# Kernel optimization log

Measured on AMD Instinct MI355X. Metric: run time of the kernel, lower is better.

Reference implementation:

```python
import jax, jax.numpy as jnp
import numpy as np

DIM = 1024
HEAD = 8
SPLIT = DIM // HEAD
EPS = 1e-6


def layernorm(x, gamma, beta):
    m = jnp.mean(x, axis=-1, keepdims=True)
    v = jnp.mean(jnp.square(x - m), axis=-1, keepdims=True)
    return (x - m) / jnp.sqrt(v + EPS) * gamma + beta


def setup_inputs() -> dict:
    key = jax.random.key(0)
    ks = jax.random.split(key, 6)
    s = 0.02
    return {
        "x": jax.random.normal(ks[0], (4, 2048, DIM), dtype=jnp.float32),
        "W_in": jax.random.normal(ks[1], (DIM, DIM), dtype=jnp.float32) * s,
        "gamma": jnp.ones((DIM,), jnp.float32),
        "beta": jnp.zeros((DIM,), jnp.float32),
        "Wq": jax.random.normal(ks[2], (HEAD, SPLIT, SPLIT), dtype=jnp.float32) * s,
        "Wk": jax.random.normal(ks[3], (HEAD, SPLIT, SPLIT), dtype=jnp.float32) * s,
        "Wv": jax.random.normal(ks[4], (HEAD, SPLIT, SPLIT), dtype=jnp.float32) * s,
        "Wf": jax.random.normal(ks[5], (DIM, DIM), dtype=jnp.float32) * s,
        "bf": jnp.zeros((DIM,), jnp.float32),
    }


def reference(x, W_in, gamma, beta, Wq, Wk, Wv, Wf, bf):
    B, S, _ = x.shape
    mod = x @ W_in  # [B,S,DIM], Dense no bias
    # pre-norm then split into heads: [B,S,HEAD,SPLIT]
    h = layernorm(mod, gamma, beta).reshape(B, S, HEAD, SPLIT)
    # per-head Q/K/V projections (batched over heads instead of Python loop)
    q = jnp.einsum('bshd,hde->bhse', h, Wq)
    k = jnp.einsum('bshd,hde->bhse', h, Wk)
    v = jnp.einsum('bshd,hde->bhse', h, Wv)
    # keras Attention(): unscaled dot-product scores (use_scale=False)
    scores = jnp.einsum('bhqe,bhke->bhqk', q, k)
    attn = jax.nn.softmax(scores, axis=-1)
    o = jnp.einsum('bhqk,bhke->bqhe', attn, v).reshape(B, S, DIM)
    mod = mod + o  # residual
    # FFN residual with shared LayerNorm params and ELU Dense
    mod = mod + jax.nn.elu(layernorm(mod, gamma, beta) @ Wf + bf)
    return mod
```

## Files before the change

kernel.cpp:

```cpp
#include <hip/hip_runtime.h>
#include <hip/hip_bf16.h>

#define DIMN 1024
#define NHEAD 8
#define ESPL 128
#define NB 4
#define SEQ 2048
#define NROWS (NB * SEQ)
#define LNEPS 1e-6f
#define L2E 1.442695041f

typedef unsigned short u16;
typedef unsigned int u32;
typedef __attribute__((ext_vector_type(8))) short short8;
typedef __attribute__((ext_vector_type(4))) short s16x4;
typedef __attribute__((ext_vector_type(4))) float f32x4;

__device__ __forceinline__ u16 f2bf(float f) {
  u32 u = __float_as_uint(f);
  u += 0x7FFFu + ((u >> 16) & 1u);
  return (u16)(u >> 16);
}

__device__ __forceinline__ u32 pk2bf(float a, float b) {
  u32 r;
  asm("v_cvt_pk_bf16_f32 %0, %1, %2" : "=v"(r) : "v"(a), "v"(b));
  return r;
}

__device__ __forceinline__ uint2 pack4bf(float4 v) {
  uint2 r;
  r.x = pk2bf(v.x, v.y);
  r.y = pk2bf(v.z, v.w);
  return r;
}

__device__ __forceinline__ float fexp2(float x) {
  float r;
  asm("v_exp_f32 %0, %1" : "=v"(r) : "v"(x));
  return r;
}

__device__ __forceinline__ float eluf(float x) { return x > 0.f ? x : expm1f(x); }

__device__ __forceinline__ void gl2lds16(const u16* g, u16* l) {
  __builtin_amdgcn_global_load_lds((const __attribute__((address_space(1))) u32*)g,
                                   (__attribute__((address_space(3))) u32*)l, 16, 0, 0);
}

__global__ __launch_bounds__(256) void ln_apply(const float* __restrict__ modp,
                                                const float* __restrict__ gamma,
                                                const float* __restrict__ beta,
                                                const float* __restrict__ s1p,
                                                const float* __restrict__ s2p,
                                                u16* __restrict__ outb) {
  int base = (blockIdx.x * 256 + threadIdx.x) * 4;
  int row = base >> 10, col = base & 1023;
  float s1 = s1p[row], s2 = s2p[row];
  float mu = s1 * (1.f / DIMN);
  float rsd = rsqrtf(fmaxf(s2 * (1.f / DIMN) - mu * mu, 0.f) + LNEPS);
  float4 v = *(const float4*)(modp + base);
  float4 g = *(const float4*)(gamma + col);
  float4 bb = *(const float4*)(beta + col);
  v.x = (v.x - mu) * rsd * g.x + bb.x;
  v.y = (v.y - mu) * rsd * g.y + bb.y;
  v.z = (v.z - mu) * rsd * g.z + bb.z;
  v.w = (v.w - mu) * rsd * g.w + bb.w;
  *(uint2*)(outb + base) = pack4bf(v);
}

__device__ __forceinline__ void wtrans_body(u16 (*tl)[68], const float* __restrict__ src,
                                            u16* __restrict__ dst, int K, int N, int n0,
                                            int k0) {
  const int t = threadIdx.x;
  const int r = t >> 2;
#pragma unroll
  for (int j = 0; j < 4; j++) {
    int f = (t & 3) + j * 4;
    float4 v = *(const float4*)(src + (size_t)(k0 + r) * N + n0 + f * 4);
    *(uint2*)&tl[r][f * 4] = pack4bf(v);
  }
  __syncthreads();
#pragma unroll
  for (int j = 0; j < 4; j++) {
    int f = (t & 3) + j * 4;
    ushort4 o;
    o.x = tl[f * 4 + 0][r];
    o.y = tl[f * 4 + 1][r];
    o.z = tl[f * 4 + 2][r];
    o.w = tl[f * 4 + 3][r];
    *(ushort4*)(dst + (size_t)(n0 + r) * K + k0 + f * 4) = o;
  }
}

__global__ __launch_bounds__(256) void prep_fused(
    const float* __restrict__ x, u16* __restrict__ xb, const float* __restrict__ W_in,
    u16* __restrict__ wt1, const float* __restrict__ Wf, u16* __restrict__ wt2,
    const float* __restrict__ Wq, const float* __restrict__ Wk, const float* __restrict__ Wv,
    u16* __restrict__ dq, u16* __restrict__ dk, u16* __restrict__ dv) {
  __shared__ u16 tl[64][68];
  const int bid = blockIdx.x;
  if (bid < NROWS) {
    int base = (bid * 256 + threadIdx.x) * 4;
    *(uint2*)(xb + base) = pack4bf(*(const float4*)(x + base));
  } else if (bid < NROWS + 512) {
    int z = bid - NROWS;
    const float* s = (z & 256) ? Wf : W_in;
    u16* d = (z & 256) ? wt2 : wt1;
    z &= 255;
    wtrans_body(tl, s, d, DIMN, DIMN, (z & 15) * 64, (z >> 4) * 64);
  } else {
    int z = bid - NROWS - 512;
    int xy = z & 3, zz = z >> 2;
    int mi = zz >> 3, hh = zz & 7;
    const float* s = (mi == 0) ? Wq : (mi == 1) ? Wk : Wv;
    u16* d = (mi == 0) ? dq : (mi == 1) ? dk : dv;
    s += (size_t)hh * ESPL * ESPL;
    d += (size_t)hh * ESPL * ESPL;
    wtrans_body(tl, s, d, ESPL, ESPL, (xy & 1) * 64, (xy >> 1) * 64);
  }
}

template <int MODE>
__global__ __launch_bounds__(256, 2) void gemm_bf16(
    const u16* __restrict__ A, const u16* __restrict__ Bt, const float* __restrict__ resid,
    const float* __restrict__ bias, float* __restrict__ s1p, float* __restrict__ s2p,
    float* __restrict__ C) {
  __shared__ __align__(16) char lds[65536];
  const int t = threadIdx.x;
  const int w = t >> 6, lane = t & 63, quad = lane >> 4, l16 = lane & 15;
  const int wm = w & 1, wn = w >> 1;
  const int lin = blockIdx.x + gridDim.x * blockIdx.y;
  const int xcd = lin & 7, slot = lin >> 3;
  const int m0 = (xcd * 8 + (slot >> 3)) * 128;
  const int n0 = (slot & 7) * 128;

  auto stage = [&](int koff, int bi) {
    const u16* ag = A + (size_t)m0 * DIMN + koff;
    const u16* bg = Bt + (size_t)n0 * DIMN + koff;
    u16* As = (u16*)(lds + bi * 32768);
    u16* Bs = (u16*)(lds + bi * 32768 + 16384);
#pragma unroll
    for (int i = 0; i < 4; i++) {
      int pbase = (w * 4 + i) * 64;
      int p = pbase + lane;
      int r = p >> 3, c8 = (p & 7) ^ (r & 7);
      gl2lds16(ag + (size_t)r * DIMN + c8 * 8, As + pbase * 8);
      gl2lds16(bg + (size_t)r * DIMN + c8 * 8, Bs + pbase * 8);
    }
  };

  f32x4 acc[4][4];
#pragma unroll
  for (int mt = 0; mt < 4; mt++)
#pragma unroll
    for (int nt = 0; nt < 4; nt++) acc[mt][nt] = (f32x4){0.f, 0.f, 0.f, 0.f};

  stage(0, 0);
  __syncthreads();
  for (int kt = 0; kt < DIMN / 64; kt++) {
    if (kt + 1 < DIMN / 64) stage((kt + 1) * 64, (kt + 1) & 1);
    const u16* As = (const u16*)(lds + (kt & 1) * 32768);
    const u16* Bs = (const u16*)(lds + (kt & 1) * 32768 + 16384);
#pragma unroll
    for (int ks = 0; ks < 2; ks++) {
      short8 af[4], bfr[4];
#pragma unroll
      for (int mt = 0; mt < 4; mt++) {
        int row = wm * 64 + mt * 16 + l16;
        int pc = (ks * 4 + quad) ^ (row & 7);
        af[mt] = *(const short8*)(As + row * 64 + pc * 8);
      }
#pragma unroll
      for (int nt = 0; nt < 4; nt++) {
        int row = wn * 64 + nt * 16 + l16;
        int pc = (ks * 4 + quad) ^ (row & 7);
        bfr[nt] = *(const short8*)(Bs + row * 64 + pc * 8);
      }
#pragma unroll
      for (int mt = 0; mt < 4; mt++)
#pragma unroll
        for (int nt = 0; nt < 4; nt++)
          acc[mt][nt] = __builtin_amdgcn_mfma_f32_16x16x32_bf16(bfr[nt], af[mt], acc[mt][nt], 0, 0, 0);
    }
    __syncthreads();
  }
#pragma unroll
  for (int mt = 0; mt < 4; mt++) {
    int row = m0 + wm * 64 + mt * 16 + l16;
    float s1 = 0.f, s2 = 0.f;
#pragma unroll
    for (int nt = 0; nt < 4; nt++) {
      int col = n0 + wn * 64 + nt * 16 + quad * 4;
      size_t off = (size_t)row * DIMN + col;
      f32x4 v = acc[mt][nt];
      if (MODE == 0) {
        *(f32x4*)(C + off) = v;
        s1 += (v[0] + v[1]) + (v[2] + v[3]);
        s2 += (v[0] * v[0] + v[1] * v[1]) + (v[2] * v[2] + v[3] * v[3]);
      } else {
        float4 rv = *(const float4*)(resid + off);
        float4 bv = *(const float4*)(bias + col);
        float4 o;
        o.x = rv.x + eluf(v[0] + bv.x);
        o.y = rv.y + eluf(v[1] + bv.y);
        o.z = rv.z + eluf(v[2] + bv.z);
        o.w = rv.w + eluf(v[3] + bv.w);
        *(float4*)(C + off) = o;
      }
    }
    if (MODE == 0) {
      s1 += __shfl_xor(s1, 16);
      s1 += __shfl_xor(s1, 32);
      s2 += __shfl_xor(s2, 16);
      s2 += __shfl_xor(s2, 32);
      if (quad == 0) {
        atomicAdd(s1p + row, s1);
        atomicAdd(s2p + row, s2);
      }
    }
  }
}

#define QP 136

__global__ __launch_bounds__(256) void qkv_mfma(
    const float* __restrict__ modp, const u16* __restrict__ wqt, const u16* __restrict__ wkt,
    const u16* __restrict__ wvt, const float* __restrict__ gamma, const float* __restrict__ beta,
    const float* __restrict__ s1p, const float* __restrict__ s2p, u16* __restrict__ qo,
    u16* __restrict__ ko, u16* __restrict__ vto) {
  __shared__ u16 Asl[128 * QP];
  __shared__ u16 Bsl[128 * QP];
  const int t = threadIdx.x;
  const int w = t >> 6, lane = t & 63, quad = lane >> 4, l16 = lane & 15;
  const int wm = w & 1, wn = w >> 1;
  const int lin = blockIdx.x + gridDim.x * blockIdx.y;
  const int xcd = lin & 7, slot = lin >> 3;
  const int s0 = (slot >> 2) * 128;
  const int bh = (slot & 3) * 8 + xcd;
  const int b = bh >> 3, hh = bh & 7;
  const int sr8 = t >> 3, sf8 = t & 7;
#pragma unroll
  for (int p = 0; p < 4; p++) {
    int r = sr8 + 32 * p;
    int rowg = b * SEQ + s0 + r;
    float s1 = s1p[rowg], s2 = s2p[rowg];
    float mu = s1 * (1.f / DIMN);
    float rsd = rsqrtf(fmaxf(s2 * (1.f / DIMN) - mu * mu, 0.f) + LNEPS);
    const float* ap = modp + (size_t)rowg * DIMN + hh * ESPL;
#pragma unroll
    for (int j = 0; j < 4; j++) {
      int f = sf8 + j * 8;
      float4 v = *(const float4*)(ap + f * 4);
      float4 g = *(const float4*)(gamma + hh * ESPL + f * 4);
      float4 bb = *(const float4*)(beta + hh * ESPL + f * 4);
      v.x = (v.x - mu) * rsd * g.x + bb.x;
      v.y = (v.y - mu) * rsd * g.y + bb.y;
      v.z = (v.z - mu) * rsd * g.z + bb.z;
      v.w = (v.w - mu) * rsd * g.w + bb.w;
      *(uint2*)(Asl + r * QP + f * 4) = pack4bf(v);
    }
  }
  __syncthreads();
  short8 afr[4][4];
#pragma unroll
  for (int k4 = 0; k4 < 4; k4++)
#pragma unroll
    for (int mt = 0; mt < 4; mt++)
      afr[k4][mt] = *(const short8*)(Asl + (wm * 64 + mt * 16 + l16) * QP + k4 * 32 + quad * 8);

  const u16* Ws[3] = {wqt, wkt, wvt};
  for (int mi = 0; mi < 3; mi++) {
    __syncthreads();
    const u16* wsrc = Ws[mi] + ((size_t)hh << 14);
#pragma unroll
    for (int p = 0; p < 4; p++) {
      int r = sr8 + 32 * p;
#pragma unroll
      for (int j = 0; j < 2; j++) {
        int f = sf8 + j * 8;
        *(uint4*)(Bsl + r * QP + f * 8) = *(const uint4*)(wsrc + r * ESPL + f * 8);
      }
    }
    __syncthreads();
    f32x4 acc[4][4];
#pragma unroll
    for (int mt = 0; mt < 4; mt++)
#pragma unroll
      for (int nt = 0; nt < 4; nt++) acc[mt][nt] = (f32x4){0.f, 0.f, 0.f, 0.f};
#pragma unroll
    for (int k4 = 0; k4 < 4; k4++) {
      short8 bfr[4];
#pragma unroll
      for (int nt = 0; nt < 4; nt++)
        bfr[nt] = *(const short8*)(Bsl + (wn * 64 + nt * 16 + l16) * QP + k4 * 32 + quad * 8);
      if (mi < 2) {
#pragma unroll
        for (int mt = 0; mt < 4; mt++)
#pragma unroll
          for (int nt = 0; nt < 4; nt++)
            acc[mt][nt] = __builtin_amdgcn_mfma_f32_16x16x32_bf16(bfr[nt], afr[k4][mt], acc[mt][nt], 0, 0, 0);
      } else {
#pragma unroll
        for (int mt = 0; mt < 4; mt++)
#pragma unroll
          for (int nt = 0; nt < 4; nt++)
            acc[mt][nt] = __builtin_amdgcn_mfma_f32_16x16x32_bf16(afr[k4][mt], bfr[nt], acc[mt][nt], 0, 0, 0);
      }
    }
    if (mi < 2) {
      u16* o = (mi == 0) ? qo : ko;
#pragma unroll
      for (int mt = 0; mt < 4; mt++) {
        int s = s0 + wm * 64 + mt * 16 + l16;
#pragma unroll
        for (int nt = 0; nt < 4; nt++) {
          int e0 = wn * 64 + nt * 16 + quad * 4;
          uint2 pk;
          pk.x = pk2bf(acc[mt][nt][0], acc[mt][nt][1]);
          pk.y = pk2bf(acc[mt][nt][2], acc[mt][nt][3]);
          *(uint2*)(o + ((size_t)bh * SEQ + s) * ESPL + e0) = pk;
        }
      }
    } else {
#pragma unroll
      for (int mt = 0; mt < 4; mt++)
#pragma unroll
        for (int nt = 0; nt < 4; nt++) {
          int e = wn * 64 + nt * 16 + l16;
          int sbase = s0 + wm * 64 + mt * 16 + quad * 4;
          uint2 pk;
          pk.x = pk2bf(acc[mt][nt][0], acc[mt][nt][1]);
          pk.y = pk2bf(acc[mt][nt][2], acc[mt][nt][3]);
          *(uint2*)(vto + ((size_t)bh * ESPL + e) * SEQ + sbase) = pk;
        }
    }
  }
}

#define OBP 132
#define RESCALE_THR 8.f

__global__ __launch_bounds__(256, 2) void attn_mfma(const u16* __restrict__ q,
                                                    const u16* __restrict__ kk,
                                                    const u16* __restrict__ vt,
                                                    float* __restrict__ modp,
                                                    float* __restrict__ s1p,
                                                    float* __restrict__ s2p) {
  __shared__ __align__(16) char lds[81920];
  const int t = threadIdx.x;
  const int w = t >> 6, lane = t & 63, quad = lane >> 4, l16 = lane & 15;
  const int lin = blockIdx.x + gridDim.x * blockIdx.y;
  const int xcd = lin & 7, slot = lin >> 3;
  const int qt = slot & 15;
  const int bh = xcd * 4 + (slot >> 4);
  const int b = bh >> 3, hh = bh & 7;
  const size_t qkbase = (size_t)bh * SEQ * ESPL;
  const int qrow0 = qt * 128 + w * 32;
  const u16* kg0 = kk + qkbase;
  const u16* vg0 = vt + qkbase;
  char* Pt = lds + 65536 + w * 4096;
  const int swz = (l16 & 7) << 4;

  short8 qf[2][4];
#pragma unroll
  for (int g = 0; g < 2; g++) {
    const u16* qrow = q + qkbase + (size_t)(qrow0 + g * 16 + l16) * ESPL + quad * 8;
#pragma unroll
    for (int kc = 0; kc < 4; kc++) qf[g][kc] = *(const short8*)(qrow + kc * 32);
  }

  float m_st[2] = {-1e30f, -1e30f}, l_st[2] = {0.f, 0.f};
  f32x4 oacc[2][8];
#pragma unroll
  for (int g = 0; g < 2; g++)
#pragma unroll
    for (int et = 0; et < 8; et++) oacc[g][et] = (f32x4){0.f, 0.f, 0.f, 0.f};

  auto stage = [&](int kt, int bi) {
    const u16* kg = kg0 + (size_t)kt * 64 * ESPL;
    const u16* vg = vg0 + (size_t)kt * 64;
    u16* Ksb = (u16*)(lds + bi * 32768);
    u16* Vsb = (u16*)(lds + bi * 32768 + 16384);
#pragma unroll
    for (int i = 0; i < 4; i++) {
      int pbase = w * 64 + i * 256;
      int p = pbase + lane;
      int r = p >> 4, c8 = (p & 15) ^ (r & 15);
      gl2lds16(kg + r * ESPL + c8 * 8, Ksb + pbase * 8);
      int e = p >> 3, v8 = (p & 7) ^ (e & 7);
      gl2lds16(vg + (size_t)e * SEQ + v8 * 8, Vsb + pbase * 8);
    }
  };

  stage(0, 0);
  __syncthreads();

  for (int kt = 0; kt < SEQ / 64; kt++) {
    if (kt + 1 < SEQ / 64) stage(kt + 1, (kt + 1) & 1);
    const u16* Ks = (const u16*)(lds + (kt & 1) * 32768);
    const u16* Vs = (const u16*)(lds + (kt & 1) * 32768 + 16384);
    f32x4 sacc[4][2];
#pragma unroll
    for (int mt = 0; mt < 4; mt++)
#pragma unroll
      for (int g = 0; g < 2; g++) sacc[mt][g] = (f32x4){0.f, 0.f, 0.f, 0.f};
    __builtin_amdgcn_s_setprio(1);
#pragma unroll
    for (int mt = 0; mt < 4; mt++) {
#pragma unroll
      for (int kc = 0; kc < 4; kc++) {
        short8 kf = *(const short8*)(Ks + (mt * 16 + l16) * 128 + (((kc * 4 + quad) ^ l16) << 3));
        sacc[mt][0] = __builtin_amdgcn_mfma_f32_16x16x32_bf16(kf, qf[0][kc], sacc[mt][0], 0, 0, 0);
        sacc[mt][1] = __builtin_amdgcn_mfma_f32_16x16x32_bf16(kf, qf[1][kc], sacc[mt][1], 0, 0, 0);
      }
    }
    __builtin_amdgcn_s_setprio(0);
    float alpha[2];
    bool updf[2];
#pragma unroll
    for (int g = 0; g < 2; g++) {
      const f32x4 a = sacc[0][g], b2 = sacc[1][g], c2 = sacc[2][g], d2 = sacc[3][g];
      float t0 = fmaxf(fmaxf(a[0], a[1]), a[2]);
      float t1 = fmaxf(fmaxf(a[3], b2[0]), b2[1]);
      float t2 = fmaxf(fmaxf(b2[2], b2[3]), c2[0]);
      float t3 = fmaxf(fmaxf(c2[1], c2[2]), c2[3]);
      float t4 = fmaxf(fmaxf(d2[0], d2[1]), d2[2]);
      float mloc = fmaxf(fmaxf(fmaxf(t0, t1), t2), fmaxf(fmaxf(t3, t4), d2[3]));
      mloc = fmaxf(mloc, __shfl_xor(mloc, 16));
      mloc = fmaxf(mloc, __shfl_xor(mloc, 32));
      updf[g] = !__all(mloc - m_st[g] <= RESCALE_THR);
      if (updf[g]) {
        float mnew = fmaxf(m_st[g], mloc);
        alpha[g] = fexp2((m_st[g] - mnew) * L2E);
        m_st[g] = mnew;
      } else {
        alpha[g] = 1.f;
      }
      const float mkn = -m_st[g] * L2E;
      float sum = 0.f;
#pragma unroll
      for (int mt = 0; mt < 4; mt++) {
        float p0 = fexp2(fmaf(sacc[mt][g][0], L2E, mkn));
        float p1 = fexp2(fmaf(sacc[mt][g][1], L2E, mkn));
        float p2 = fexp2(fmaf(sacc[mt][g][2], L2E, mkn));
        float p3 = fexp2(fmaf(sacc[mt][g][3], L2E, mkn));
        sum += (p0 + p1) + (p2 + p3);
        uint2 pkv = make_uint2(pk2bf(p0, p1), pk2bf(p2, p3));
        *(uint2*)(Pt + g * 2048 + l16 * 128 + ((mt * 32 + quad * 8) ^ swz)) = pkv;
      }
      sum += __shfl_xor(sum, 16);
      sum += __shfl_xor(sum, 32);
      l_st[g] = l_st[g] * alpha[g] + sum;
    }
    if (updf[0]) {
#pragma unroll
      for (int et = 0; et < 8; et++)
#pragma unroll
        for (int r = 0; r < 4; r++) oacc[0][et][r] *= alpha[0];
    }
    if (updf[1]) {
#pragma unroll
      for (int et = 0; et < 8; et++)
#pragma unroll
        for (int r = 0; r < 4; r++) oacc[1][et][r] *= alpha[1];
    }
    short8 pb[2][2];
#pragma unroll
    for (int g = 0; g < 2; g++)
#pragma unroll
      for (int mtp = 0; mtp < 2; mtp++)
        pb[g][mtp] = *(const short8*)(Pt + g * 2048 + l16 * 128 + ((mtp * 64 + quad * 16) ^ swz));
    __builtin_amdgcn_s_setprio(1);
#pragma unroll
    for (int et = 0; et < 8; et++) {
#pragma unroll
      for (int mtp = 0; mtp < 2; mtp++) {
        short8 vf8 = *(const short8*)(Vs + (size_t)(et * 16 + l16) * 64 +
                                      (((mtp * 4 + quad) ^ (l16 & 7)) << 3));
        oacc[0][et] = __builtin_amdgcn_mfma_f32_16x16x32_bf16(vf8, pb[0][mtp], oacc[0][et], 0, 0, 0);
        oacc[1][et] = __builtin_amdgcn_mfma_f32_16x16x32_bf16(vf8, pb[1][mtp], oacc[1][et], 0, 0, 0);
      }
    }
    __builtin_amdgcn_s_setprio(0);
    __syncthreads();
  }

  float* Obuf = (float*)lds;
  {
    float linv[2] = {1.f / l_st[0], 1.f / l_st[1]};
    float* Ow = Obuf + (size_t)w * 32 * OBP;
#pragma unroll
    for (int g = 0; g < 2; g++)
#pragma unroll
      for (int et = 0; et < 8; et++) {
        f32x4 ov = oacc[g][et];
        ov[0] *= linv[g];
        ov[1] *= linv[g];
        ov[2] *= linv[g];
        ov[3] *= linv[g];
        *(f32x4*)(Ow + (size_t)(g * 16 + l16) * OBP + et * 16 + quad * 4) = ov;
      }
  }
  __syncthreads();
  const int rr = t >> 3, cc = (t & 7) << 4;
  for (int c = 0; c < 4; c++) {
    int qglob = qt * 128 + c * 32 + rr;
    float* mp = modp + ((size_t)(b * SEQ + qglob)) * DIMN + hh * ESPL + cc;
    const float* Oc = Obuf + (size_t)c * 32 * OBP + (size_t)rr * OBP + cc;
    float s1 = 0.f, s2 = 0.f;
#pragma unroll
    for (int j = 0; j < 4; j++) {
      float4 ov = *(const float4*)(Oc + j * 4);
      float4 mv = *(const float4*)(mp + j * 4);
      mv.x += ov.x;
      mv.y += ov.y;
      mv.z += ov.z;
      mv.w += ov.w;
      *(float4*)(mp + j * 4) = mv;
      s1 += (mv.x + mv.y) + (mv.z + mv.w);
      s2 += (mv.x * mv.x + mv.y * mv.y) + (mv.z * mv.z + mv.w * mv.w);
    }
    s1 += __shfl_xor(s1, 1);
    s1 += __shfl_xor(s1, 2);
    s1 += __shfl_xor(s1, 4);
    s2 += __shfl_xor(s2, 1);
    s2 += __shfl_xor(s2, 2);
    s2 += __shfl_xor(s2, 4);
    if ((t & 7) == 0) {
      atomicAdd(s1p + b * SEQ + qglob, s1);
      atomicAdd(s2p + b * SEQ + qglob, s2);
    }
  }
}

extern "C" void kernel_launch(void* const* d_in, const int* in_sizes, int n_in, void* d_out,
                              int out_size, void* d_ws, size_t ws_size, hipStream_t stream) {
  (void)in_sizes;
  (void)n_in;
  (void)out_size;
  (void)ws_size;
  const float* x = (const float*)d_in[0];
  const float* W_in = (const float*)d_in[1];
  const float* gamma = (const float*)d_in[2];
  const float* beta = (const float*)d_in[3];
  const float* Wq = (const float*)d_in[4];
  const float* Wk = (const float*)d_in[5];
  const float* Wv = (const float*)d_in[6];
  const float* Wf = (const float*)d_in[7];
  const float* bf = (const float*)d_in[8];
  float* out = (float*)d_out;

  char* ws = (char*)d_ws;
  const size_t MB = 1024ull * 1024;
  float* mod = (float*)ws;
  u16* qb = (u16*)(ws + 32 * MB);
  u16* kb = (u16*)(ws + 48 * MB);
  u16* vtb = (u16*)(ws + 64 * MB);
  float* sums = (float*)(ws + 80 * MB);
  float* s1a = sums;
  float* s2a = s1a + NROWS;
  float* s1b = s2a + NROWS;
  float* s2b = s1b + NROWS;
  u16* wqt = (u16*)(ws + 80 * MB + 4 * NROWS * sizeof(float));
  u16* wkt = wqt + NHEAD * ESPL * ESPL;
  u16* wvt = wkt + NHEAD * ESPL * ESPL;
  u16* wt2 = wvt + NHEAD * ESPL * ESPL;
  u16* wt1 = qb;
  u16* xb = kb;
  u16* modb = qb;

  hipMemsetAsync(sums, 0, 4 * NROWS * sizeof(float), stream);
  prep_fused<<<NROWS + 512 + 96, 256, 0, stream>>>(x, xb, W_in, wt1, Wf, wt2, Wq, Wk, Wv, wqt,
                                                   wkt, wvt);

  dim3 gg(DIMN / 128, NROWS / 128);
  gemm_bf16<0><<<gg, 256, 0, stream>>>(xb, wt1, nullptr, nullptr, s1a, s2a, mod);
  qkv_mfma<<<dim3(SEQ / 128, NB * NHEAD), 256, 0, stream>>>(mod, wqt, wkt, wvt, gamma, beta,
                                                            s1a, s2a, qb, kb, vtb);
  attn_mfma<<<dim3(SEQ / 128, NB * NHEAD), 256, 0, stream>>>(qb, kb, vtb, mod, s1b, s2b);
  ln_apply<<<NROWS * DIMN / 1024, 256, 0, stream>>>(mod, gamma, beta, s1b, s2b, modb);
  gemm_bf16<1><<<gg, 256, 0, stream>>>(modb, wt2, mod, bf, nullptr, nullptr, out);
}
```

Baseline: 296.7 us.

## Split attention block into eight waves of sixteen query rows each

Restructures the attention kernel so each 128-query tile is handled by 8 waves of 16 rows instead of 4 waves of 32 rows, with 512 threads per block. It halves per-wave accumulator and Q-fragment registers and spreads K/V staging across more waves. The trade-off is that each K/V LDS fragment now feeds one MFMA instead of two, doubling shared-memory reads per unit of work. The epilogue is reworked so each row is written back by four threads.

```diff
diff --git a/kernel.cpp b/kernel.cpp
--- a/kernel.cpp
+++ b/kernel.cpp
@@ -341,7 +341,7 @@
 #define OBP 132
 #define RESCALE_THR 8.f
 
-__global__ __launch_bounds__(256, 2) void attn_mfma(const u16* __restrict__ q,
+__global__ __launch_bounds__(512, 4) void attn_mfma(const u16* __restrict__ q,
                                                     const u16* __restrict__ kk,
                                                     const u16* __restrict__ vt,
                                                     float* __restrict__ modp,
@@ -356,26 +356,23 @@
   const int bh = xcd * 4 + (slot >> 4);
   const int b = bh >> 3, hh = bh & 7;
   const size_t qkbase = (size_t)bh * SEQ * ESPL;
-  const int qrow0 = qt * 128 + w * 32;
+  const int qrow0 = qt * 128 + w * 16;
   const u16* kg0 = kk + qkbase;
   const u16* vg0 = vt + qkbase;
-  char* Pt = lds + 65536 + w * 4096;
+  char* Pt = lds + 65536 + w * 2048;
   const int swz = (l16 & 7) << 4;
 
-  short8 qf[2][4];
-#pragma unroll
-  for (int g = 0; g < 2; g++) {
-    const u16* qrow = q + qkbase + (size_t)(qrow0 + g * 16 + l16) * ESPL + quad * 8;
-#pragma unroll
-    for (int kc = 0; kc < 4; kc++) qf[g][kc] = *(const short8*)(qrow + kc * 32);
-  }
-
-  float m_st[2] = {-1e30f, -1e30f}, l_st[2] = {0.f, 0.f};
-  f32x4 oacc[2][8];
-#pragma unroll
-  for (int g = 0; g < 2; g++)
-#pragma unroll
-    for (int et = 0; et < 8; et++) oacc[g][et] = (f32x4){0.f, 0.f, 0.f, 0.f};
+  short8 qf[4];
+  {
+    const u16* qrow = q + qkbase + (size_t)(qrow0 + l16) * ESPL + quad * 8;
+#pragma unroll
+    for (int kc = 0; kc < 4; kc++) qf[kc] = *(const short8*)(qrow + kc * 32);
+  }
+
+  float m_st = -1e30f, l_st = 0.f;
+  f32x4 oacc[8];
+#pragma unroll
+  for (int et = 0; et < 8; et++) oacc[et] = (f32x4){0.f, 0.f, 0.f, 0.f};
 
   auto stage = [&](int kt, int bi) {
     const u16* kg = kg0 + (size_t)kt * 64 * ESPL;
@@ -383,8 +380,8 @@
     u16* Ksb = (u16*)(lds + bi * 32768);
     u16* Vsb = (u16*)(lds + bi * 32768 + 16384);
 #pragma unroll
-    for (int i = 0; i < 4; i++) {
-      int pbase = w * 64 + i * 256;
+    for (int i = 0; i < 2; i++) {
+      int pbase = w * 128 + i * 64;
       int p = pbase + lane;
       int r = p >> 4, c8 = (p & 15) ^ (r & 15);
       gl2lds16(kg + r * ESPL + c8 * 8, Ksb + pbase * 8);
@@ -400,27 +397,21 @@
     if (kt + 1 < SEQ / 64) stage(kt + 1, (kt + 1) & 1);
     const u16* Ks = (const u16*)(lds + (kt & 1) * 32768);
     const u16* Vs = (const u16*)(lds + (kt & 1) * 32768 + 16384);
-    f32x4 sacc[4][2];
-#pragma unroll
-    for (int mt = 0; mt < 4; mt++)
-#pragma unroll
-      for (int g = 0; g < 2; g++) sacc[mt][g] = (f32x4){0.f, 0.f, 0.f, 0.f};
+    f32x4 sacc[4];
+#pragma unroll
+    for (int mt = 0; mt < 4; mt++) sacc[mt] = (f32x4){0.f, 0.f, 0.f, 0.f};
     __builtin_amdgcn_s_setprio(1);
 #pragma unroll
     for (int mt = 0; mt < 4; mt++) {
 #pragma unroll
       for (int kc = 0; kc < 4; kc++) {
         short8 kf = *(const short8*)(Ks + (mt * 16 + l16) * 128 + (((kc * 4 + quad) ^ l16) << 3));
-        sacc[mt][0] = __builtin_amdgcn_mfma_f32_16x16x32_bf16(kf, qf[0][kc], sacc[mt][0], 0, 0, 0);
-        sacc[mt][1] = __builtin_amdgcn_mfma_f32_16x16x32_bf16(kf, qf[1][kc], sacc[mt][1], 0, 0, 0);
+        sacc[mt] = __builtin_amdgcn_mfma_f32_16x16x32_bf16(kf, qf[kc], sacc[mt], 0, 0, 0);
       }
     }
     __builtin_amdgcn_s_setprio(0);
-    float alpha[2];
-    bool updf[2];
-#pragma unroll
-    for (int g = 0; g < 2; g++) {
-      const f32x4 a = sacc[0][g], b2 = sacc[1][g], c2 = sacc[2][g], d2 = sacc[3][g];
+    {
+      const f32x4 a = sacc[0], b2 = sacc[1], c2 = sacc[2], d2 = sacc[3];
       float t0 = fmaxf(fmaxf(a[0], a[1]), a[2]);
       float t1 = fmaxf(fmaxf(a[3], b2[0]), b2[1]);
       float t2 = fmaxf(fmaxf(b2[2], b2[3]), c2[0]);
@@ -429,48 +420,39 @@
       float mloc = fmaxf(fmaxf(fmaxf(t0, t1), t2), fmaxf(fmaxf(t3, t4), d2[3]));
       mloc = fmaxf(mloc, __shfl_xor(mloc, 16));
       mloc = fmaxf(mloc, __shfl_xor(mloc, 32));
-      updf[g] = !__all(mloc - m_st[g] <= RESCALE_THR);
-      if (updf[g]) {
-        float mnew = fmaxf(m_st[g], mloc);
-        alpha[g] = fexp2((m_st[g] - mnew) * L2E);
-        m_st[g] = mnew;
-      } else {
-        alpha[g] = 1.f;
-      }
-      const float mkn = -m_st[g] * L2E;
+      bool updf = !__all(mloc - m_st <= RESCALE_THR);
+      float alpha = 1.f;
+      if (updf) {
+        float mnew = fmaxf(m_st, mloc);
+        alpha = fexp2((m_st - mnew) * L2E);
+        m_st = mnew;
+      }
+      const float mkn = -m_st * L2E;
       float sum = 0.f;
 #pragma unroll
       for (int mt = 0; mt < 4; mt++) {
-        float p0 = fexp2(fmaf(sacc[mt][g][0], L2E, mkn));
-        float p1 = fexp2(fmaf(sacc[mt][g][1], L2E, mkn));
-        float p2 = fexp2(fmaf(sacc[mt][g][2], L2E, mkn));
-        float p3 = fexp2(fmaf(sacc[mt][g][3], L2E, mkn));
+        float p0 = fexp2(fmaf(sacc[mt][0], L2E, mkn));
+        float p1 = fexp2(fmaf(sacc[mt][1], L2E, mkn));
+        float p2 = fexp2(fmaf(sacc[mt][2], L2E, mkn));
+        float p3 = fexp2(fmaf(sacc[mt][3], L2E, mkn));
         sum += (p0 + p1) + (p2 + p3);
         uint2 pkv = make_uint2(pk2bf(p0, p1), pk2bf(p2, p3));
-        *(uint2*)(Pt + g * 2048 + l16 * 128 + ((mt * 32 + quad * 8) ^ swz)) = pkv;
+        *(uint2*)(Pt + l16 * 128 + ((mt * 32 + quad * 8) ^ swz)) = pkv;
       }
       sum += __shfl_xor(sum, 16);
       sum += __shfl_xor(sum, 32);
-      l_st[g] = l_st[g] * alpha[g] + sum;
-    }
-    if (updf[0]) {
-#pragma unroll
-      for (int et = 0; et < 8; et++)
-#pragma unroll
-        for (int r = 0; r < 4; r++) oacc[0][et][r] *= alpha[0];
-    }
-    if (updf[1]) {
-#pragma unroll
-      for (int et = 0; et < 8; et++)
-#pragma unroll
-        for (int r = 0; r < 4; r++) oacc[1][et][r] *= alpha[1];
-    }
-    short8 pb[2][2];
-#pragma unroll
-    for (int g = 0; g < 2; g++)
-#pragma unroll
-      for (int mtp = 0; mtp < 2; mtp++)
-        pb[g][mtp] = *(const short8*)(Pt + g * 2048 + l16 * 128 + ((mtp * 64 + quad * 16) ^ swz));
+      l_st = l_st * alpha + sum;
+      if (updf) {
+#pragma unroll
+        for (int et = 0; et < 8; et++)
+#pragma unroll
+          for (int r = 0; r < 4; r++) oacc[et][r] *= alpha;
+      }
+    }
+    short8 pb[2];
+#pragma unroll
+    for (int mtp = 0; mtp < 2; mtp++)
+      pb[mtp] = *(const short8*)(Pt + l16 * 128 + ((mtp * 64 + quad * 16) ^ swz));
     __builtin_amdgcn_s_setprio(1);
 #pragma unroll
     for (int et = 0; et < 8; et++) {
@@ -478,8 +460,7 @@
       for (int mtp = 0; mtp < 2; mtp++) {
         short8 vf8 = *(const short8*)(Vs + (size_t)(et * 16 + l16) * 64 +
                                       (((mtp * 4 + quad) ^ (l16 & 7)) << 3));
-        oacc[0][et] = __builtin_amdgcn_mfma_f32_16x16x32_bf16(vf8, pb[0][mtp], oacc[0][et], 0, 0, 0);
-        oacc[1][et] = __builtin_amdgcn_mfma_f32_16x16x32_bf16(vf8, pb[1][mtp], oacc[1][et], 0, 0, 0);
+        oacc[et] = __builtin_amdgcn_mfma_f32_16x16x32_bf16(vf8, pb[mtp], oacc[et], 0, 0, 0);
       }
     }
     __builtin_amdgcn_s_setprio(0);
@@ -488,49 +469,43 @@
 
   float* Obuf = (float*)lds;
   {
-    float linv[2] = {1.f / l_st[0], 1.f / l_st[1]};
-    float* Ow = Obuf + (size_t)w * 32 * OBP;
-#pragma unroll
-    for (int g = 0; g < 2; g++)
-#pragma unroll
-      for (int et = 0; et < 8; et++) {
-        f32x4 ov = oacc[g][et];
-        ov[0] *= linv[g];
-        ov[1] *= linv[g];
-        ov[2] *= linv[g];
-        ov[3] *= linv[g];
-        *(f32x4*)(Ow + (size_t)(g * 16 + l16) * OBP + et * 16 + quad * 4) = ov;
-      }
+    float linv = 1.f / l_st;
+    float* Ow = Obuf + (size_t)w * 16 * OBP;
+#pragma unroll
+    for (int et = 0; et < 8; et++) {
+      f32x4 ov = oacc[et];
+      ov[0] *= linv;
+      ov[1] *= linv;
+      ov[2] *= linv;
+      ov[3] *= linv;
+      *(f32x4*)(Ow + (size_t)l16 * OBP + et * 16 + quad * 4) = ov;
+    }
   }
   __syncthreads();
-  const int rr = t >> 3, cc = (t & 7) << 4;
-  for (int c = 0; c < 4; c++) {
-    int qglob = qt * 128 + c * 32 + rr;
-    float* mp = modp + ((size_t)(b * SEQ + qglob)) * DIMN + hh * ESPL + cc;
-    const float* Oc = Obuf + (size_t)c * 32 * OBP + (size_t)rr * OBP + cc;
-    float s1 = 0.f, s2 = 0.f;
-#pragma unroll
-    for (int j = 0; j < 4; j++) {
-      float4 ov = *(const float4*)(Oc + j * 4);
-      float4 mv = *(const float4*)(mp + j * 4);
-      mv.x += ov.x;
-      mv.y += ov.y;
-      mv.z += ov.z;
-      mv.w += ov.w;
-      *(float4*)(mp + j * 4) = mv;
-      s1 += (mv.x + mv.y) + (mv.z + mv.w);
-      s2 += (mv.x * mv.x + mv.y * mv.y) + (mv.z * mv.z + mv.w * mv.w);
-    }
-    s1 += __shfl_xor(s1, 1);
-    s1 += __shfl_xor(s1, 2);
-    s1 += __shfl_xor(s1, 4);
-    s2 += __shfl_xor(s2, 1);
-    s2 += __shfl_xor(s2, 2);
-    s2 += __shfl_xor(s2, 4);
-    if ((t & 7) == 0) {
-      atomicAdd(s1p + b * SEQ + qglob, s1);
-      atomicAdd(s2p + b * SEQ + qglob, s2);
-    }
+  const int rr = t >> 2, cc = (t & 3) << 5;
+  int qglob = qt * 128 + rr;
+  float* mp = modp + ((size_t)(b * SEQ + qglob)) * DIMN + hh * ESPL + cc;
+  const float* Oc = Obuf + (size_t)rr * OBP + cc;
+  float s1 = 0.f, s2 = 0.f;
+#pragma unroll
+  for (int j = 0; j < 8; j++) {
+    float4 ov = *(const float4*)(Oc + j * 4);
+    float4 mv = *(const float4*)(mp + j * 4);
+    mv.x += ov.x;
+    mv.y += ov.y;
+    mv.z += ov.z;
+    mv.w += ov.w;
+    *(float4*)(mp + j * 4) = mv;
+    s1 += (mv.x + mv.y) + (mv.z + mv.w);
+    s2 += (mv.x * mv.x + mv.y * mv.y) + (mv.z * mv.z + mv.w * mv.w);
+  }
+  s1 += __shfl_xor(s1, 1);
+  s1 += __shfl_xor(s1, 2);
+  s2 += __shfl_xor(s2, 1);
+  s2 += __shfl_xor(s2, 2);
+  if ((t & 3) == 0) {
+    atomicAdd(s1p + b * SEQ + qglob, s1);
+    atomicAdd(s2p + b * SEQ + qglob, s2);
   }
 }
 
@@ -578,7 +553,7 @@
   gemm_bf16<0><<<gg, 256, 0, stream>>>(xb, wt1, nullptr, nullptr, s1a, s2a, mod);
   qkv_mfma<<<dim3(SEQ / 128, NB * NHEAD), 256, 0, stream>>>(mod, wqt, wkt, wvt, gamma, beta,
                                                             s1a, s2a, qb, kb, vtb);
-  attn_mfma<<<dim3(SEQ / 128, NB * NHEAD), 256, 0, stream>>>(qb, kb, vtb, mod, s1b, s2b);
+  attn_mfma<<<dim3(SEQ / 128, NB * NHEAD), 512, 0, stream>>>(qb, kb, vtb, mod, s1b, s2b);
   ln_apply<<<NROWS * DIMN / 1024, 256, 0, stream>>>(mod, gamma, beta, s1b, s2b, modb);
   gemm_bf16<1><<<gg, 256, 0, stream>>>(modb, wt2, mod, bf, nullptr, nullptr, out);
 }
```

Result: faster. 288.2 us (-2.9%).

## Use 256-query attention blocks with 8 waves and write output directly from registers

Applied to the files above, without the earlier changes.

The attention kernel now launches 512-thread blocks that each cover 256 query rows with 8 waves. Each K/V tile staged in LDS is therefore shared by twice as many queries, halving global K/V traffic per query. The epilogue drops the LDS transpose buffer and adds the normalized accumulators straight into the residual, reducing row sums with lane shuffles. The trade-off is a larger LDS footprint (96KB) and 512-thread blocks, which may lower occupancy. The direct stores are also less coalesced, since each lane writes 16-byte pieces spread across many rows.

```diff
diff --git a/kernel.cpp b/kernel.cpp
--- a/kernel.cpp
+++ b/kernel.cpp
@@ -338,25 +338,24 @@
   }
 }
 
-#define OBP 132
 #define RESCALE_THR 8.f
 
-__global__ __launch_bounds__(256, 2) void attn_mfma(const u16* __restrict__ q,
+__global__ __launch_bounds__(512, 2) void attn_mfma(const u16* __restrict__ q,
                                                     const u16* __restrict__ kk,
                                                     const u16* __restrict__ vt,
                                                     float* __restrict__ modp,
                                                     float* __restrict__ s1p,
                                                     float* __restrict__ s2p) {
-  __shared__ __align__(16) char lds[81920];
+  __shared__ __align__(16) char lds[98304];
   const int t = threadIdx.x;
   const int w = t >> 6, lane = t & 63, quad = lane >> 4, l16 = lane & 15;
   const int lin = blockIdx.x + gridDim.x * blockIdx.y;
   const int xcd = lin & 7, slot = lin >> 3;
-  const int qt = slot & 15;
-  const int bh = xcd * 4 + (slot >> 4);
+  const int qt = slot & 7;
+  const int bh = xcd * 4 + (slot >> 3);
   const int b = bh >> 3, hh = bh & 7;
   const size_t qkbase = (size_t)bh * SEQ * ESPL;
-  const int qrow0 = qt * 128 + w * 32;
+  const int qrow0 = qt * 256 + w * 32;
   const u16* kg0 = kk + qkbase;
   const u16* vg0 = vt + qkbase;
   char* Pt = lds + 65536 + w * 4096;
@@ -383,8 +382,8 @@
     u16* Ksb = (u16*)(lds + bi * 32768);
     u16* Vsb = (u16*)(lds + bi * 32768 + 16384);
 #pragma unroll
-    for (int i = 0; i < 4; i++) {
-      int pbase = w * 64 + i * 256;
+    for (int i = 0; i < 2; i++) {
+      int pbase = w * 128 + i * 64;
       int p = pbase + lane;
       int r = p >> 4, c8 = (p & 15) ^ (r & 15);
       gl2lds16(kg + r * ESPL + c8 * 8, Ksb + pbase * 8);
@@ -486,48 +485,30 @@
     __syncthreads();
   }
 
-  float* Obuf = (float*)lds;
-  {
-    float linv[2] = {1.f / l_st[0], 1.f / l_st[1]};
-    float* Ow = Obuf + (size_t)w * 32 * OBP;
-#pragma unroll
-    for (int g = 0; g < 2; g++)
-#pragma unroll
-      for (int et = 0; et < 8; et++) {
-        f32x4 ov = oacc[g][et];
-        ov[0] *= linv[g];
-        ov[1] *= linv[g];
-        ov[2] *= linv[g];
-        ov[3] *= linv[g];
-        *(f32x4*)(Ow + (size_t)(g * 16 + l16) * OBP + et * 16 + quad * 4) = ov;
-      }
-  }
-  __syncthreads();
-  const int rr = t >> 3, cc = (t & 7) << 4;
-  for (int c = 0; c < 4; c++) {
-    int qglob = qt * 128 + c * 32 + rr;
-    float* mp = modp + ((size_t)(b * SEQ + qglob)) * DIMN + hh * ESPL + cc;
-    const float* Oc = Obuf + (size_t)c * 32 * OBP + (size_t)rr * OBP + cc;
+#pragma unroll
+  for (int g = 0; g < 2; g++) {
+    float linv = 1.f / l_st[g];
+    int qglob = qrow0 + g * 16 + l16;
+    float* mp = modp + ((size_t)(b * SEQ + qglob)) * DIMN + hh * ESPL;
     float s1 = 0.f, s2 = 0.f;
 #pragma unroll
-    for (int j = 0; j < 4; j++) {
-      float4 ov = *(const float4*)(Oc + j * 4);
-      float4 mv = *(const float4*)(mp + j * 4);
-      mv.x += ov.x;
-      mv.y += ov.y;
-      mv.z += ov.z;
-      mv.w += ov.w;
-      *(float4*)(mp + j * 4) = mv;
+    for (int et = 0; et < 8; et++) {
+      int e0 = et * 16 + quad * 4;
+      f32x4 ov = oacc[g][et];
+      float4 mv = *(const float4*)(mp + e0);
+      mv.x += ov[0] * linv;
+      mv.y += ov[1] * linv;
+      mv.z += ov[2] * linv;
+      mv.w += ov[3] * linv;
+      *(float4*)(mp + e0) = mv;
       s1 += (mv.x + mv.y) + (mv.z + mv.w);
       s2 += (mv.x * mv.x + mv.y * mv.y) + (mv.z * mv.z + mv.w * mv.w);
     }
-    s1 += __shfl_xor(s1, 1);
-    s1 += __shfl_xor(s1, 2);
-    s1 += __shfl_xor(s1, 4);
-    s2 += __shfl_xor(s2, 1);
-    s2 += __shfl_xor(s2, 2);
-    s2 += __shfl_xor(s2, 4);
-    if ((t & 7) == 0) {
+    s1 += __shfl_xor(s1, 16);
+    s1 += __shfl_xor(s1, 32);
+    s2 += __shfl_xor(s2, 16);
+    s2 += __shfl_xor(s2, 32);
+    if (quad == 0) {
       atomicAdd(s1p + b * SEQ + qglob, s1);
       atomicAdd(s2p + b * SEQ + qglob, s2);
     }
@@ -578,7 +559,7 @@
   gemm_bf16<0><<<gg, 256, 0, stream>>>(xb, wt1, nullptr, nullptr, s1a, s2a, mod);
   qkv_mfma<<<dim3(SEQ / 128, NB * NHEAD), 256, 0, stream>>>(mod, wqt, wkt, wvt, gamma, beta,
                                                             s1a, s2a, qb, kb, vtb);
-  attn_mfma<<<dim3(SEQ / 128, NB * NHEAD), 256, 0, stream>>>(qb, kb, vtb, mod, s1b, s2b);
+  attn_mfma<<<dim3(SEQ / 256, NB * NHEAD), 512, 0, stream>>>(qb, kb, vtb, mod, s1b, s2b);
   ln_apply<<<NROWS * DIMN / 1024, 256, 0, stream>>>(mod, gamma, beta, s1b, s2b, modb);
   gemm_bf16<1><<<gg, 256, 0, stream>>>(modb, wt2, mod, bf, nullptr, nullptr, out);
 }
```

Result: faster. 284.9 us (-4.0%).
